# Kernel optimization log

Hardware: AMD Instinct MI355X
Metric: run time of the kernel (lower is better)

## Reference

```python
import jax, jax.numpy as jnp
import numpy as np

# Tier config (cumulative d_model [256,1024,2048], cumulative heads [4,12,24], d_k=64)
TIER_OWN = [256, 768, 1024]      # per-tier own hidden dims
HEAD_OUT = [256, 512, 768]       # n_heads_per_tier[i] * d_k
NHS = [4, 8, 12]
DKS = [64, 64, 64]
RANK = 8
IN_OFF = np.cumsum([0] + TIER_OWN)    # [0,256,1024,2048]
OUT_OFF = np.cumsum([0] + HEAD_OUT)   # [0,256,768,1536]


def _block_ut_weight(key, in_dims, out_dims):
    """Full (sum_in, sum_out) matrix with lower-triangular blocks zeroed."""
    io = np.cumsum([0] + list(in_dims))
    oo = np.cumsum([0] + list(out_dims))
    n = len(in_dims)
    mask = np.zeros((io[-1], oo[-1]), dtype=np.float32)
    for i in range(n):
        for j in range(i, n):
            mask[io[i]:io[i + 1], oo[j]:oo[j + 1]] = 1.0
    W = jax.random.normal(key, (io[-1], oo[-1]), dtype=jnp.float32) * 0.02
    return W * jnp.asarray(mask)


def setup_inputs() -> dict:
    key = jax.random.key(0)
    ks = jax.random.split(key, 16)
    B, T, D = 4, 1024, 2048
    x = jax.random.normal(ks[0], (B, T, D), dtype=jnp.float32)
    W_Q = _block_ut_weight(ks[1], TIER_OWN, HEAD_OUT)
    W_K = _block_ut_weight(ks[2], TIER_OWN, HEAD_OUT)
    W_V = _block_ut_weight(ks[3], TIER_OWN, HEAD_OUT)
    W_O = _block_ut_weight(ks[4], HEAD_OUT, TIER_OWN)
    # feedback for tiers 0 and 1 (tier 2 has no higher tiers)
    hi0 = TIER_OWN[1] + TIER_OWN[2]  # 1792
    hi1 = TIER_OWN[2]                # 1024
    FK0 = jax.random.normal(ks[5], (hi0, NHS[0] * RANK), dtype=jnp.float32) * 0.02
    PK0 = jax.random.normal(ks[6], (NHS[0], RANK, DKS[0]), dtype=jnp.float32) * 0.01
    FV0 = jax.random.normal(ks[7], (hi0, NHS[0] * RANK), dtype=jnp.float32) * 0.02
    PV0 = jax.random.normal(ks[8], (NHS[0], RANK, DKS[0]), dtype=jnp.float32) * 0.01
    FK1 = jax.random.normal(ks[9], (hi1, NHS[1] * RANK), dtype=jnp.float32) * 0.02
    PK1 = jax.random.normal(ks[10], (NHS[1], RANK, DKS[1]), dtype=jnp.float32) * 0.01
    FV1 = jax.random.normal(ks[11], (hi1, NHS[1] * RANK), dtype=jnp.float32) * 0.02
    PV1 = jax.random.normal(ks[12], (NHS[1], RANK, DKS[1]), dtype=jnp.float32) * 0.01
    return dict(x=x, W_Q=W_Q, W_K=W_K, W_V=W_V, W_O=W_O,
                FK0=FK0, PK0=PK0, FV0=FV0, PV0=PV0,
                FK1=FK1, PK1=PK1, FV1=FV1, PV1=PV1)


def _forward(x, W_Q, W_K, W_V, W_O, FK0, PK0, FV0, PV0, FK1, PK1, FV1, PV1):
    B, T, _ = x.shape
    Q_all = x @ W_Q
    K_all = x @ W_K
    V_all = x @ W_V
    causal = jnp.tril(jnp.ones((T, T), dtype=bool))
    fb = {0: (FK0, PK0, FV0, PV0), 1: (FK1, PK1, FV1, PV1)}
    head_outs = []
    for tier in range(3):
        nh, dk = NHS[tier], DKS[tier]
        dim = nh * dk
        o = int(OUT_OFF[tier])
        Q = Q_all[..., o:o + dim]
        K = K_all[..., o:o + dim]
        V = V_all[..., o:o + dim]
        if tier in fb:
            Fk, Pk, Fv, Pv = fb[tier]
            h_hi = x[..., int(IN_OFF[tier + 1]):]  # higher tiers' hidden
            c_k = (h_hi @ Fk).reshape(B, T, nh, RANK)
            K = K + jnp.einsum('bthr,hrd->bthd', c_k, Pk).reshape(B, T, dim)
            c_v = (h_hi @ Fv).reshape(B, T, nh, RANK)
            V = V + jnp.einsum('bthr,hrd->bthd', c_v, Pv).reshape(B, T, dim)
        Qh = Q.reshape(B, T, nh, dk).transpose(0, 2, 1, 3)
        Kh = K.reshape(B, T, nh, dk).transpose(0, 2, 1, 3)
        Vh = V.reshape(B, T, nh, dk).transpose(0, 2, 1, 3)
        scores = jnp.einsum('bhqd,bhkd->bhqk', Qh, Kh) / jnp.sqrt(jnp.float32(dk))
        scores = jnp.where(causal, scores, jnp.float32(-1e30))
        attn = jax.nn.softmax(scores, axis=-1)
        out = jnp.einsum('bhqk,bhkd->bhqd', attn, Vh)
        head_outs.append(out.transpose(0, 2, 1, 3).reshape(B, T, dim))
    return jnp.concatenate(head_outs, axis=-1) @ W_O


def reference(x, W_Q, W_K, W_V, W_O, FK0, PK0, FV0, PV0, FK1, PK1, FV1, PV1):
    return _forward(x, W_Q, W_K, W_V, W_O, FK0, PK0, FV0, PV0, FK1, PK1, FV1, PV1)
```

## Files before the change

kernel.cpp:

```cpp
#include <hip/hip_runtime.h>


typedef short bf16x8 __attribute__((ext_vector_type(8)));
typedef float floatx4 __attribute__((ext_vector_type(4)));

__device__ __forceinline__ unsigned short f2bf(float f) {
  unsigned u = __builtin_bit_cast(unsigned, f);
  u += 0x7fffu + ((u >> 16) & 1u);
  return (unsigned short)(u >> 16);
}

__device__ __forceinline__ void gload_lds16(const unsigned short* g, unsigned short* l) {
  __builtin_amdgcn_global_load_lds((const __attribute__((address_space(1))) unsigned int*)g,
                                   (__attribute__((address_space(3))) unsigned int*)l, 16, 0, 0);
}

__global__ __launch_bounds__(256) void k_prep(
    const float* __restrict__ x, unsigned short* __restrict__ X16,
    const float* __restrict__ WQ, const float* __restrict__ WK, const float* __restrict__ WV,
    const float* __restrict__ FK0, const float* __restrict__ PK0,
    const float* __restrict__ FV0, const float* __restrict__ PV0,
    const float* __restrict__ FK1, const float* __restrict__ PK1,
    const float* __restrict__ FV1, const float* __restrict__ PV1,
    unsigned short* __restrict__ WTQKV,
    const float* __restrict__ WO, unsigned short* __restrict__ WTO) {
  __shared__ float tile[32][33];
  __shared__ float Fs[32][9];
  __shared__ float Ps[8][32];
  const int bid = blockIdx.x;
  const int tid = threadIdx.x;
  if (bid < 8192) {
    int i = bid * 256 + tid;
    float4 v = ((const float4*)x)[i];
    uint2 o;
    asm("v_cvt_pk_bf16_f32 %0, %1, %2" : "=v"(o.x) : "v"(v.x), "v"(v.y));
    asm("v_cvt_pk_bf16_f32 %0, %1, %2" : "=v"(o.y) : "v"(v.z), "v"(v.w));
    ((uint2*)X16)[i] = o;
    return;
  }
  const int tx = tid & 31, ty = tid >> 5;
  if (bid < 17408) {
    int t = bid - 8192;
    int k0 = (t & 63) * 32, n0 = (t >> 6) * 32;
    const float* src; int nboff;
    if (n0 < 1536)      { src = WQ; nboff = n0; }
    else if (n0 < 3072) { src = WK; nboff = n0 - 1536; }
    else                { src = WV; nboff = n0 - 3072; }
#pragma unroll
    for (int j = 0; j < 4; ++j) {
      int kk = ty + j * 8;
      tile[kk][tx] = src[(size_t)(k0 + kk) * 1536 + nboff + tx];
    }
    int corrsel = 0; const float* Fsrc = nullptr; const float* Psrc = nullptr;
    int h = 0, d0 = 0, fs = 0, koff = 0;
    if (n0 >= 1536) {
      bool isK = (n0 < 3072);
      int np0 = isK ? (n0 - 1536) : (n0 - 3072);
      if (np0 < 256) {
        if (k0 >= 256) { corrsel = 1; Fsrc = isK ? FK0 : FV0; Psrc = isK ? PK0 : PV0;
                         h = np0 >> 6; d0 = np0 & 63; fs = 32; koff = k0 - 256; }
      } else if (np0 < 768) {
        if (k0 >= 1024) { corrsel = 1; Fsrc = isK ? FK1 : FV1; Psrc = isK ? PK1 : PV1;
                          h = (np0 - 256) >> 6; d0 = (np0 - 256) & 63; fs = 64; koff = k0 - 1024; }
      }
    }
    if (corrsel) {
      Fs[tid >> 3][tid & 7] = Fsrc[(size_t)(koff + (tid >> 3)) * fs + h * 8 + (tid & 7)];
      Ps[tid >> 5][tid & 31] = Psrc[h * 512 + (tid >> 5) * 64 + d0 + (tid & 31)];
    }
    __syncthreads();
    const float qscale = (n0 < 1536) ? 0.18033688f : 1.0f;
#pragma unroll
    for (int j = 0; j < 4; ++j) {
      int nn = ty + j * 8;
      float v = tile[tx][nn];
      if (corrsel) {
        float c = 0.f;
#pragma unroll
        for (int r = 0; r < 8; ++r) c += Fs[tx][r] * Ps[r][nn];
        v += c;
      }
      WTQKV[(size_t)(n0 + nn) * 2048 + k0 + tx] = f2bf(v * qscale);
    }
  } else {
    int t = bid - 17408;
    int k0 = (t % 48) * 32, n0 = (t / 48) * 32;
#pragma unroll
    for (int j = 0; j < 4; ++j)
      tile[ty + j * 8][tx] = WO[(size_t)(k0 + ty + j * 8) * 2048 + n0 + tx];
    __syncthreads();
#pragma unroll
    for (int j = 0; j < 4; ++j)
      WTO[(size_t)(n0 + ty + j * 8) * 1536 + k0 + tx] = f2bf(tile[tx][ty + j * 8]);
  }
}

template <bool OUT_BF16, int MODE>
__global__ __launch_bounds__(256) void k_gemm_bt(const unsigned short* __restrict__ A,
                                                 const unsigned short* __restrict__ Bt,
                                                 void* __restrict__ C, int M, int N, int K,
                                                 unsigned short* __restrict__ VTout) {
  __shared__ unsigned short As[128 * 64];
  __shared__ unsigned short Bs[128 * 64];
  const int tid = threadIdx.x;
  const int wave = tid >> 6, lane = tid & 63;
  const int qd = lane >> 4, ln = lane & 15;
  const int idx = blockIdx.x;
  const int xcd = idx & 7, r = idx >> 3;
  int bx, by;
  if (MODE == 0) {
    if (r < 120) {
      int L = xcd * 120 + r;
      int scol = L / 192, q = L % 192;
      by = q / 6; bx = 6 + (4 - scol) * 6 + q % 6;
    } else {
      int ms = xcd * 24 + (r - 120);
      if (ms < 128) { bx = 2 + (ms & 3); by = ms >> 2; }
      else          { int sh = ms - 128; bx = sh & 1; by = sh >> 1; }
    }
  } else {
    if (r < 32) {
      int L = xcd * 32 + r;
      int scol = L >> 7, q = L & 127;
      by = q >> 2; bx = 8 + scol * 4 + (q & 3);
    } else if (r < 56) {
      int m = xcd * 24 + (r - 32);
      bx = 2 + m % 6; by = m / 6;
    } else {
      int sh = xcd * 8 + (r - 56);
      bx = sh & 1; by = sh >> 1;
    }
  }
  const int bm = by * 128, bn = bx * 128;
  const int wr = wave >> 1, wc = wave & 1;
  int Keff;
  if (MODE == 0) Keff = (bn < 256) ? 256 : (bn < 768 ? 1024 : 2048);
  else           Keff = (bn < 256) ? 256 : (bn < 1024 ? 768 : 1536);
  floatx4 acc[4][4];
#pragma unroll
  for (int i = 0; i < 4; ++i)
#pragma unroll
    for (int j = 0; j < 4; ++j) acc[i][j] = (floatx4){0.f, 0.f, 0.f, 0.f};
  const int rl = lane >> 3;
  const int sg = (lane & 7) ^ rl;
  const unsigned short* gA = A + (size_t)(bm + wave * 32 + rl) * K + sg * 8;
  const unsigned short* gB = Bt + (size_t)(bn + wave * 32 + rl) * K + sg * 8;
  unsigned short* lA = As + wave * 2048;
  unsigned short* lB = Bs + wave * 2048;
  const int l7 = ln & 7;
  for (int k0 = 0; k0 < Keff; k0 += 64) {
    __syncthreads();
#pragma unroll
    for (int i = 0; i < 4; ++i) {
      gload_lds16(gA + (size_t)8 * i * K + k0, lA + i * 512);
      gload_lds16(gB + (size_t)8 * i * K + k0, lB + i * 512);
    }
    __syncthreads();
#pragma unroll
    for (int h = 0; h < 2; ++h) {
      bf16x8 af[4], bfr[4];
#pragma unroll
      for (int mi = 0; mi < 4; ++mi)
        af[mi] = *(const bf16x8*)(As + (wr * 64 + mi * 16 + ln) * 64 + ((h * 4 + qd) ^ l7) * 8);
#pragma unroll
      for (int ni = 0; ni < 4; ++ni)
        bfr[ni] = *(const bf16x8*)(Bs + (wc * 64 + ni * 16 + ln) * 64 + ((h * 4 + qd) ^ l7) * 8);
#pragma unroll
      for (int mi = 0; mi < 4; ++mi)
#pragma unroll
        for (int ni = 0; ni < 4; ++ni)
          acc[mi][ni] = __builtin_amdgcn_mfma_f32_16x16x32_bf16(af[mi], bfr[ni], acc[mi][ni], 0, 0, 0);
    }
  }
  if (MODE == 0 && bn >= 3072) {
    __syncthreads();
    unsigned short* tw = (wave < 2) ? (As + wave * 4096) : (Bs + (wave - 2) * 4096);
#pragma unroll
    for (int mi = 0; mi < 4; ++mi)
#pragma unroll
      for (int ni = 0; ni < 4; ++ni) {
        uint2 pv2;
        asm("v_cvt_pk_bf16_f32 %0, %1, %2" : "=v"(pv2.x) : "v"(acc[mi][ni][0]), "v"(acc[mi][ni][1]));
        asm("v_cvt_pk_bf16_f32 %0, %1, %2" : "=v"(pv2.y) : "v"(acc[mi][ni][2]), "v"(acc[mi][ni][3]));
        int d = ni * 16 + ln;
        int c = mi * 2 + (qd >> 1);
        *(uint2*)(tw + d * 64 + ((c ^ (ln & 7)) << 3) + ((qd & 1) << 2)) = pv2;
      }
    __asm__ volatile("s_waitcnt lgkmcnt(0)" ::: "memory");
    const int a = lane >> 3, bl = lane & 7;
    const int bb = bm >> 10, tt0 = bm & 1023;
    const int dbase = (bn - 3072) + wc * 64;
    const int tg = tt0 + wr * 64 + bl * 8;
#pragma unroll
    for (int i = 0; i < 8; ++i) {
      int d = a + 8 * i;
      uint4 v = *(const uint4*)(tw + d * 64 + ((bl ^ a) << 3));
      *(uint4*)(VTout + ((size_t)(bb * 1536 + dbase + d)) * 1024 + tg) = v;
    }
  } else {
#pragma unroll
    for (int mi = 0; mi < 4; ++mi)
#pragma unroll
      for (int r2 = 0; r2 < 4; ++r2) {
        int row = bm + wr * 64 + mi * 16 + qd * 4 + r2;
#pragma unroll
        for (int ni = 0; ni < 4; ++ni) {
          int col = bn + wc * 64 + ni * 16 + ln;
          if (OUT_BF16)
            ((unsigned short*)C)[(size_t)row * N + col] = f2bf(acc[mi][ni][r2]);
          else
            ((float*)C)[(size_t)row * N + col] = acc[mi][ni][r2];
        }
      }
  }
}

#define LDP 136
__global__ __launch_bounds__(256) void k_attn(const unsigned short* __restrict__ QKV,
                                              const unsigned short* __restrict__ VT,
                                              unsigned short* __restrict__ Oout) {
  __shared__ unsigned short Ks[128 * 64];
  __shared__ unsigned short VTs[64 * 128];
  __shared__ unsigned short Pl[4][16 * LDP];
  const int tid = threadIdx.x;
  const int wave = tid >> 6, lane = tid & 63;
  const int qd = lane >> 4, ln = lane & 15;
  const int gh = blockIdx.x, b = blockIdx.y;
  const int qb = 7 - (int)blockIdx.z;
  const int T = 1024, LD = 3072;
  const size_t rowbase = (size_t)b * T * LD;
  const int qcol = 64 * gh, kcol = 1536 + 64 * gh;
  const unsigned short* VTg = VT + ((size_t)b * 1536 + 64 * gh) * 1024;
  const int q0 = qb * 128 + wave * 16;

  bf16x8 aq[2][2];
#pragma unroll
  for (int j = 0; j < 2; ++j) {
    const unsigned short* qp = QKV + rowbase + (size_t)(q0 + j * 64 + ln) * LD + qcol;
    aq[j][0] = *(const bf16x8*)(qp + qd * 8);
    aq[j][1] = *(const bf16x8*)(qp + 32 + qd * 8);
  }
  floatx4 Oacc[2][4];
#pragma unroll
  for (int j = 0; j < 2; ++j)
#pragma unroll
    for (int i = 0; i < 4; ++i) Oacc[j][i] = (floatx4){0.f, 0.f, 0.f, 0.f};
  float l_lane[2] = {0.f, 0.f};

  const int rk = lane >> 3;
  const int gk = ((lane & 7) ^ rk) * 8;
  const unsigned short* gK = QKV + rowbase + (size_t)(wave * 32 + rk) * LD + kcol + gk;
  unsigned short* lK = Ks + wave * 32 * 64;
  const int rv = lane >> 4;
  const int cv = lane & 15;
  unsigned short* lV = VTs + wave * 16 * 128;
  const unsigned short* gVrow[4];
  int gvcol[4];
#pragma unroll
  for (int i = 0; i < 4; ++i) {
    int d = wave * 16 + 4 * i + rv;
    gVrow[i] = VTg + (size_t)d * 1024;
    gvcol[i] = (cv ^ (4 * i + rv)) * 8;
  }
  const int l7 = ln & 7;

  bf16x8 kr[4], vr[4];
#pragma unroll
  for (int i = 0; i < 4; ++i) {
    kr[i] = *(const bf16x8*)(gK + (size_t)(8 * i) * LD);
    vr[i] = *(const bf16x8*)(gVrow[i] + gvcol[i]);
  }

  for (int jt = 0; jt <= qb; ++jt) {
    const int jk = jt * 128;
    const bool diag = (jt == qb);
    __syncthreads();
#pragma unroll
    for (int i = 0; i < 4; ++i) {
      *(bf16x8*)(lK + i * 512 + lane * 8) = kr[i];
      *(bf16x8*)(lV + i * 512 + lane * 8) = vr[i];
    }
    __syncthreads();
    if (jt < qb) {
      const int nk = jk + 128;
#pragma unroll
      for (int i = 0; i < 4; ++i) {
        kr[i] = *(const bf16x8*)(gK + (size_t)(nk + 8 * i) * LD);
        vr[i] = *(const bf16x8*)(gVrow[i] + nk + gvcol[i]);
      }
    }

#pragma unroll
    for (int j = 0; j < 2; ++j) {
      const bool dj0 = diag && (j == 0);
      const int hmax = dj0 ? 4 : 8;
      floatx4 Sc[8];
#pragma unroll
      for (int h = 0; h < 8; ++h) {
        if (h >= hmax) continue;
        Sc[h] = (floatx4){0.f, 0.f, 0.f, 0.f};
        bf16x8 a0 = *(const bf16x8*)(Ks + (h * 16 + ln) * 64 + (qd ^ l7) * 8);
        bf16x8 a1 = *(const bf16x8*)(Ks + (h * 16 + ln) * 64 + ((4 + qd) ^ l7) * 8);
        Sc[h] = __builtin_amdgcn_mfma_f32_16x16x32_bf16(a0, aq[j][0], Sc[h], 0, 0, 0);
        Sc[h] = __builtin_amdgcn_mfma_f32_16x16x32_bf16(a1, aq[j][1], Sc[h], 0, 0, 0);
      }
      const int qrow = q0 + j * 64 + ln;
      unsigned short* pw = Pl[wave];
#pragma unroll
      for (int h = 0; h < 8; ++h) {
        if (h >= hmax) continue;
        float pv[4];
#pragma unroll
        for (int r = 0; r < 4; ++r) {
          float p = __builtin_amdgcn_exp2f(fminf(Sc[h][r], 80.f));
          if (diag && (j == 0 || h >= 4)) {
            int key = jk + h * 16 + qd * 4 + r;
            if (key > qrow) p = 0.f;
          }
          l_lane[j] += p;
          pv[r] = p;
        }
        uint2 pk2;
        asm("v_cvt_pk_bf16_f32 %0, %1, %2" : "=v"(pk2.x) : "v"(pv[0]), "v"(pv[1]));
        asm("v_cvt_pk_bf16_f32 %0, %1, %2" : "=v"(pk2.y) : "v"(pv[2]), "v"(pv[3]));
        *(uint2*)(pw + ln * LDP + h * 16 + qd * 4) = pk2;
      }
      __asm__ volatile("s_waitcnt lgkmcnt(0)" ::: "memory");
      const int smax = dj0 ? 2 : 4;
      bf16x8 pa[4];
#pragma unroll
      for (int s = 0; s < 4; ++s) {
        if (s >= smax) continue;
        pa[s] = *(const bf16x8*)(pw + ln * LDP + s * 32 + qd * 8);
      }
#pragma unroll
      for (int nc = 0; nc < 4; ++nc) {
        const int d = nc * 16 + ln;
#pragma unroll
        for (int s = 0; s < 4; ++s) {
          if (s >= smax) continue;
          bf16x8 bv = *(const bf16x8*)(VTs + d * 128 + (((s * 4 + qd) ^ ln) & 15) * 8);
          Oacc[j][nc] = __builtin_amdgcn_mfma_f32_16x16x32_bf16(pa[s], bv, Oacc[j][nc], 0, 0, 0);
        }
      }
    }
  }
#pragma unroll
  for (int j = 0; j < 2; ++j) {
    float l = l_lane[j];
    l += __shfl_xor(l, 16, 64);
    l += __shfl_xor(l, 32, 64);
#pragma unroll
    for (int r = 0; r < 4; ++r) {
      float inv = 1.0f / __shfl(l, qd * 4 + r, 64);
      size_t row = (size_t)b * T + q0 + j * 64 + qd * 4 + r;
#pragma unroll
      for (int nc = 0; nc < 4; ++nc)
        Oout[row * 1536 + 64 * gh + nc * 16 + ln] = f2bf(Oacc[j][nc][r] * inv);
    }
  }
}

extern "C" void kernel_launch(void* const* d_in, const int* in_sizes, int n_in,
                              void* d_out, int out_size, void* d_ws, size_t ws_size,
                              hipStream_t stream) {
  (void)in_sizes; (void)n_in; (void)out_size; (void)ws_size;
  const float* x   = (const float*)d_in[0];
  const float* WQ  = (const float*)d_in[1];
  const float* WK  = (const float*)d_in[2];
  const float* WV  = (const float*)d_in[3];
  const float* WO  = (const float*)d_in[4];
  const float* FK0 = (const float*)d_in[5];
  const float* PK0 = (const float*)d_in[6];
  const float* FV0 = (const float*)d_in[7];
  const float* PV0 = (const float*)d_in[8];
  const float* FK1 = (const float*)d_in[9];
  const float* PK1 = (const float*)d_in[10];
  const float* FV1 = (const float*)d_in[11];
  const float* PV1 = (const float*)d_in[12];

  char* ws = (char*)d_ws;
  unsigned short* X16   = (unsigned short*)(ws + 0);
  unsigned short* WTQKV = (unsigned short*)(ws + 16777216);
  unsigned short* QK    = (unsigned short*)(ws + 35651584);
  unsigned short* VT    = (unsigned short*)(ws + 60817408);
  unsigned short* ATT   = (unsigned short*)(ws + 73400320);
  unsigned short* WTO   = (unsigned short*)(ws + 85983232);

  k_prep<<<20480, 256, 0, stream>>>(x, X16, WQ, WK, WV,
                                    FK0, PK0, FV0, PV0, FK1, PK1, FV1, PV1,
                                    WTQKV, WO, WTO);
  k_gemm_bt<true, 0><<<1152, 256, 0, stream>>>(X16, WTQKV, QK, 4096, 3072, 2048, VT);
  k_attn<<<dim3(24, 4, 8), 256, 0, stream>>>(QK, VT, ATT);
  k_gemm_bt<false, 1><<<512, 256, 0, stream>>>(ATT, WTO, d_out, 4096, 2048, 1536, nullptr);
}
```

Baseline: 296.3 us.

## Replace output projection GEMM with triple-buffered 64x128 tile kernel skipping zero blocks

Adds a dedicated output-projection GEMM that uses smaller 64x128 tiles, a three-stage LDS ring filled by direct global-to-LDS loads, XOR-swizzled LDS offsets, and a single barrier per k-step. Each output column block iterates only over the nonzero K range of the block-upper-triangular W_O (48, 24 or 9 steps), and blocks are assigned XCD-aware. The aim is to hide load latency, avoid work on the zero blocks, and raise occupancy with 1024 blocks. The cost is tighter synchronisation through manual vmcnt waits and uneven per-block work.

```diff
diff --git a/kernel.cpp b/kernel.cpp
--- a/kernel.cpp
+++ b/kernel.cpp
@@ -95,6 +95,11 @@
   }
 }
 
+__device__ __forceinline__ int lds_off(int row, int kq) {
+  int L = row >> 1;
+  return L * 64 + ((((row & 1) << 2) | kq) ^ (L & 7)) * 8;
+}
+
 template <bool OUT_BF16, int MODE>
 __global__ __launch_bounds__(256) void k_gemm_bt(const unsigned short* __restrict__ A,
                                                  const unsigned short* __restrict__ Bt,
@@ -215,6 +220,110 @@
   }
 }
 
+#define G2_VM3 asm volatile("s_waitcnt vmcnt(3)" ::: "memory")
+#define G2_VM0 asm volatile("s_waitcnt vmcnt(0)" ::: "memory")
+
+#define G2_STEP(AP, BP, AQ, BQ, STG, K2, FINQ)                                  \
+  do {                                                                          \
+    bf16x8 af[4], bfr[2];                                                       \
+    _Pragma("unroll")                                                           \
+    for (int mi = 0; mi < 4; ++mi) af[mi] = *(const bf16x8*)((AP) + aoff[mi]);  \
+    _Pragma("unroll")                                                           \
+    for (int ni = 0; ni < 2; ++ni) bfr[ni] = *(const bf16x8*)((BP) + boff[ni]); \
+    if (STG) {                                                                  \
+      gload_lds16(gAs + (K2), (AQ) + wave * 512);                               \
+      gload_lds16(gBs + (K2), (BQ) + wave * 512);                               \
+      gload_lds16(gBs + 64 * 1536 + (K2), (BQ) + 2048 + wave * 512);            \
+    }                                                                           \
+    __builtin_amdgcn_s_barrier();                                               \
+    _Pragma("unroll")                                                           \
+    for (int mi = 0; mi < 4; ++mi)                                              \
+      _Pragma("unroll")                                                         \
+      for (int ni = 0; ni < 2; ++ni)                                            \
+        acc[mi][ni] = __builtin_amdgcn_mfma_f32_16x16x32_bf16(af[mi], bfr[ni], acc[mi][ni], 0, 0, 0); \
+    if (FINQ) {                                                                 \
+      if (STG) { G2_VM3; } else { G2_VM0; }                                     \
+      __builtin_amdgcn_s_barrier();                                             \
+    }                                                                           \
+  } while (0)
+
+__global__ __launch_bounds__(256) void k_gemm2(const unsigned short* __restrict__ A,
+                                               const unsigned short* __restrict__ Bt,
+                                               float* __restrict__ C) {
+  __shared__ unsigned short As0[2048], As1[2048], As2[2048];
+  __shared__ unsigned short Bs0[4096], Bs1[4096], Bs2[4096];
+  const int tid = threadIdx.x;
+  const int wave = tid >> 6, lane = tid & 63;
+  const int qd = lane >> 4, ln = lane & 15;
+  const int idx = blockIdx.x;
+  const int xcd = idx & 7, r = idx >> 3;
+  int bx, by, NT;
+  if (r < 64) {
+    int L = xcd * 64 + r;
+    int scol = L >> 8, q = L & 255;
+    by = q >> 2; bx = 8 + scol * 4 + (q & 3);
+    NT = 48;
+  } else if (r < 112) {
+    int L = xcd * 48 + (r - 64);
+    int scol = L / 192, q = L % 192;
+    by = q / 3; bx = 2 + scol * 3 + q % 3;
+    NT = 24;
+  } else {
+    int L = xcd * 16 + (r - 112);
+    bx = L >> 6; by = L & 63;
+    NT = 9;
+  }
+  const int bm = by * 64, bn = bx * 128;
+
+  const int Lr = tid >> 3, sl = tid & 7;
+  const int gg = sl ^ (Lr & 7);
+  const int srow = 2 * Lr + (gg >> 2);
+  const int skg = gg & 3;
+  const unsigned short* gAs = A + (size_t)(bm + srow) * 1536 + skg * 8;
+  const unsigned short* gBs = Bt + (size_t)(bn + srow) * 1536 + skg * 8;
+
+  int aoff[4], boff[2];
+#pragma unroll
+  for (int mi = 0; mi < 4; ++mi) aoff[mi] = lds_off(mi * 16 + ln, qd);
+#pragma unroll
+  for (int ni = 0; ni < 2; ++ni) boff[ni] = lds_off(wave * 32 + ni * 16 + ln, qd);
+
+  floatx4 acc[4][2];
+#pragma unroll
+  for (int i = 0; i < 4; ++i)
+#pragma unroll
+    for (int j = 0; j < 2; ++j) acc[i][j] = (floatx4){0.f, 0.f, 0.f, 0.f};
+
+  gload_lds16(gAs, As0 + wave * 512);
+  gload_lds16(gBs, Bs0 + wave * 512);
+  gload_lds16(gBs + 64 * 1536, Bs0 + 2048 + wave * 512);
+  gload_lds16(gAs + 32, As1 + wave * 512);
+  gload_lds16(gBs + 32, Bs1 + wave * 512);
+  gload_lds16(gBs + 64 * 1536 + 32, Bs1 + 2048 + wave * 512);
+  G2_VM3;
+  __builtin_amdgcn_s_barrier();
+
+  const int NT3 = NT / 3;
+  for (int i = 0; i < NT3; ++i) {
+    const int t0 = 3 * i;
+    G2_STEP(As0, Bs0, As2, Bs2, (t0 + 2) < NT, (t0 + 2) * 32, (t0 + 1) < NT);
+    G2_STEP(As1, Bs1, As0, Bs0, (t0 + 3) < NT, (t0 + 3) * 32, (t0 + 2) < NT);
+    G2_STEP(As2, Bs2, As1, Bs1, (t0 + 4) < NT, (t0 + 4) * 32, (t0 + 3) < NT);
+  }
+
+#pragma unroll
+  for (int mi = 0; mi < 4; ++mi)
+#pragma unroll
+    for (int r2 = 0; r2 < 4; ++r2) {
+      size_t row = (size_t)(bm + mi * 16 + qd * 4 + r2);
+#pragma unroll
+      for (int ni = 0; ni < 2; ++ni) {
+        int col = bn + wave * 32 + ni * 16 + ln;
+        C[row * 2048 + col] = acc[mi][ni][r2];
+      }
+    }
+}
+
 #define LDP 136
 __global__ __launch_bounds__(256) void k_attn(const unsigned short* __restrict__ QKV,
                                               const unsigned short* __restrict__ VT,
@@ -392,5 +501,5 @@
                                     WTQKV, WO, WTO);
   k_gemm_bt<true, 0><<<1152, 256, 0, stream>>>(X16, WTQKV, QK, 4096, 3072, 2048, VT);
   k_attn<<<dim3(24, 4, 8), 256, 0, stream>>>(QK, VT, ATT);
-  k_gemm_bt<false, 1><<<512, 256, 0, stream>>>(ATT, WTO, d_out, 4096, 2048, 1536, nullptr);
-}
+  k_gemm2<<<1024, 256, 0, stream>>>(ATT, WTO, (float*)d_out);
+}
```

Result: no change. 300.8 us (+1.5%).
